# Optimization experiments

Measured on AMD Instinct MI355X. Metric: run time of the kernel, lower is better.

## Reference

```python
import jax, jax.numpy as jnp
import numpy as np

NUM_SUBNETS = 64
IN, HID, OUT = 6, 4, 2   # hard-coded in SubNetwork(6, 4, 2)
GHID = 6                 # GatingNetwork(6, 6, num_subnets)
BATCH = 524288


def tanhshrink(x):
    return x - jnp.tanh(x)


def setup_inputs() -> dict:
    key = jax.random.key(0)
    ks = jax.random.split(key, 9)
    s = 0.5
    return {
        "x":    jax.random.normal(ks[0], (BATCH, IN), dtype=jnp.float32),
        # stacked per-subnet params: SubNetwork layer1 (6->4), layer2 (4->2)
        "W1":   jax.random.normal(ks[1], (NUM_SUBNETS, HID, IN), dtype=jnp.float32) * s,
        "b1":   jax.random.normal(ks[2], (NUM_SUBNETS, HID), dtype=jnp.float32) * s,
        "W2":   jax.random.normal(ks[3], (NUM_SUBNETS, OUT, HID), dtype=jnp.float32) * s,
        "b2":   jax.random.normal(ks[4], (NUM_SUBNETS, OUT), dtype=jnp.float32) * s,
        # gating network: 6 -> 6 -> num_subnets
        "Gw1":  jax.random.normal(ks[5], (GHID, IN), dtype=jnp.float32) * s,
        "Gb1":  jax.random.normal(ks[6], (GHID,), dtype=jnp.float32) * s,
        "Gw2":  jax.random.normal(ks[7], (NUM_SUBNETS, GHID), dtype=jnp.float32) * s,
        "Gb2":  jax.random.normal(ks[8], (NUM_SUBNETS,), dtype=jnp.float32) * s,
    }


def reference(x, W1, b1, W2, b2, Gw1, Gb1, Gw2, Gb2):
    # All subnet MLPs fused across the subnet axis s (batched over b):
    h = tanhshrink(jnp.einsum('bi,shi->bsh', x, W1) + b1)          # [B, S, HID]
    outs = jnp.tanh(jnp.einsum('bsh,soh->bso', h, W2) + b2)       # [B, S, OUT]
    # Gating MLP; Softmax(dim=0) on an unbatched vector == softmax over subnets per sample
    g = tanhshrink(jnp.einsum('bi,hi->bh', x, Gw1) + Gb1)          # [B, GHID]
    gate = jax.nn.softmax(jnp.einsum('bh,sh->bs', g, Gw2) + Gb2, axis=-1)  # [B, S]
    # gate_weights @ outputs
    return jnp.einsum('bs,bso->bo', gate, outs)                    # [B, OUT]
```

## Files before the change

kernel.cpp:

```cpp
#include <hip/hip_runtime.h>


#define NSUB 64
#define L2E  1.4426950408889634f
#define L2E2 2.8853900817779268f

typedef float v2f __attribute__((ext_vector_type(2)));

__device__ __forceinline__ v2f pk_fma(v2f a, v2f b, v2f c) {
    return __builtin_elementwise_fma(a, b, c);
}
__device__ __forceinline__ v2f sp(float s) { return v2f{s, s}; }

__device__ __forceinline__ v2f sig_u(v2f z) {
    v2f e;
    e.x = __builtin_amdgcn_exp2f(z.x);
    e.y = __builtin_amdgcn_exp2f(z.y);
    v2f ep = e + 1.0f;
    v2f u;
    u.x = __builtin_amdgcn_rcpf(ep.x);
    u.y = __builtin_amdgcn_rcpf(ep.y);
    return u;
}

__device__ __forceinline__ float tanhshrink_s(float a) {
    float e = __builtin_amdgcn_exp2f(a * L2E2);
    float r = __builtin_amdgcn_rcpf(e + 1.0f);
    return fmaf(2.0f, r, a - 1.0f);
}

__global__ void pack_kernel(const float* __restrict__ W1, const float* __restrict__ b1,
                            const float* __restrict__ W2, const float* __restrict__ b2,
                            const float* __restrict__ Gw2, const float* __restrict__ Gb2,
                            float* __restrict__ ws)
{
    int p = threadIdx.x;
    if (p >= 32) return;
    int sa = p, sb = p + 32;
    float* f = ws + p * 128;
    for (int i = 0; i < 24; ++i) { f[2*i]   = W1[sa*24+i]*L2E2;  f[2*i+1]   = W1[sb*24+i]*L2E2; }
    for (int i = 0; i < 4;  ++i) { f[48+2*i] = b1[sa*4+i]*L2E2;  f[48+2*i+1] = b1[sb*4+i]*L2E2; }
    for (int i = 0; i < 8;  ++i) { f[56+2*i] = W2[sa*8+i];       f[56+2*i+1] = W2[sb*8+i]; }
    for (int i = 0; i < 8;  ++i) { f[72+2*i] = W2[sa*8+i]*(2.0f*L2E2);
                                   f[72+2*i+1] = W2[sb*8+i]*(2.0f*L2E2); }
    for (int o = 0; o < 2; ++o) {
        float rsA = 0.f, rsB = 0.f;
        for (int j = 0; j < 4; ++j) { rsA += W2[sa*8+o*4+j]; rsB += W2[sb*8+o*4+j]; }
        f[88+2*o]   = (b2[sa*2+o] - rsA) * L2E2;
        f[88+2*o+1] = (b2[sb*2+o] - rsB) * L2E2;
    }
    for (int i = 0; i < 6;  ++i) { f[92+2*i] = Gw2[sa*6+i]*L2E;  f[92+2*i+1] = Gw2[sb*6+i]*L2E; }
    f[104] = Gb2[sa]*L2E; f[105] = Gb2[sb]*L2E;
    for (int i = 106; i < 128; ++i) f[i] = 0.f;
}

__global__ __launch_bounds__(256) void moe_kernel(
    const float* __restrict__ x,
    const float* __restrict__ wpack,
    const float* __restrict__ Gw1, const float* __restrict__ Gb1,
    float* __restrict__ out)
{
    long t = blockIdx.x * blockDim.x + threadIdx.x;

    const float2* xv = (const float2*)(x + t * 6);
    float2 p0 = xv[0];
    float2 p1 = xv[1];
    float2 p2 = xv[2];
    float xs[6] = {p0.x, p0.y, p1.x, p1.y, p2.x, p2.y};

    float ga[6];
#pragma unroll
    for (int j = 0; j < 6; ++j) {
        float s = Gb1[j];
#pragma unroll
        for (int i = 0; i < 6; ++i)
            s = fmaf(Gw1[j * 6 + i], xs[i], s);
        ga[j] = tanhshrink_s(s);
    }

    v2f xa[6], gab[6];
#pragma unroll
    for (int i = 0; i < 6; ++i) xa[i] = sp(xs[i]);
#pragma unroll
    for (int j = 0; j < 6; ++j) gab[j] = sp(ga[j]);

    v2f accE = sp(0.f), accU0 = sp(0.f), accU1 = sp(0.f);

#pragma unroll 2
    for (int p = 0; p < 32; ++p) {
        const v2f* f2 = (const v2f*)(wpack + p * 128);

        v2f s0 = pk_fma(f2[0],  xa[0], f2[24]);
        v2f s1 = pk_fma(f2[6],  xa[0], f2[25]);
        v2f s2 = pk_fma(f2[12], xa[0], f2[26]);
        v2f s3 = pk_fma(f2[18], xa[0], f2[27]);
#pragma unroll
        for (int i = 1; i < 6; ++i) {
            s0 = pk_fma(f2[i],      xa[i], s0);
            s1 = pk_fma(f2[6 + i],  xa[i], s1);
            s2 = pk_fma(f2[12 + i], xa[i], s2);
            s3 = pk_fma(f2[18 + i], xa[i], s3);
        }

        v2f u0 = sig_u(s0);
        v2f u1 = sig_u(s1);
        v2f u2 = sig_u(s2);
        v2f u3 = sig_u(s3);

        v2f q0 = pk_fma(f2[28], s0, f2[44]);
        q0 = pk_fma(f2[29], s1, q0);
        q0 = pk_fma(f2[30], s2, q0);
        q0 = pk_fma(f2[31], s3, q0);
        q0 = pk_fma(f2[36], u0, q0);
        q0 = pk_fma(f2[37], u1, q0);
        q0 = pk_fma(f2[38], u2, q0);
        q0 = pk_fma(f2[39], u3, q0);

        v2f q1 = pk_fma(f2[32], s0, f2[45]);
        q1 = pk_fma(f2[33], s1, q1);
        q1 = pk_fma(f2[34], s2, q1);
        q1 = pk_fma(f2[35], s3, q1);
        q1 = pk_fma(f2[40], u0, q1);
        q1 = pk_fma(f2[41], u1, q1);
        q1 = pk_fma(f2[42], u2, q1);
        q1 = pk_fma(f2[43], u3, q1);

        v2f uo0 = sig_u(q0);
        v2f uo1 = sig_u(q1);

        v2f la = pk_fma(f2[46], gab[0], f2[52]);
        la = pk_fma(f2[47], gab[1], la);
        la = pk_fma(f2[48], gab[2], la);
        la = pk_fma(f2[49], gab[3], la);
        la = pk_fma(f2[50], gab[4], la);
        la = pk_fma(f2[51], gab[5], la);
        v2f ea;
        ea.x = __builtin_amdgcn_exp2f(la.x);
        ea.y = __builtin_amdgcn_exp2f(la.y);

        accE  = accE + ea;
        accU0 = pk_fma(ea, uo0, accU0);
        accU1 = pk_fma(ea, uo1, accU1);
    }

    float E  = accE.x + accE.y;
    float r  = __builtin_amdgcn_rcpf(E);
    float U0 = accU0.x + accU0.y;
    float U1 = accU1.x + accU1.y;
    float2 res;
    res.x = fmaf(-2.0f * U0, r, 1.0f);
    res.y = fmaf(-2.0f * U1, r, 1.0f);
    ((float2*)&out[t * 2])[0] = res;
}

extern "C" void kernel_launch(void* const* d_in, const int* in_sizes, int n_in,
                              void* d_out, int out_size, void* d_ws, size_t ws_size,
                              hipStream_t stream) {
    const float* x   = (const float*)d_in[0];
    const float* W1  = (const float*)d_in[1];
    const float* b1  = (const float*)d_in[2];
    const float* W2  = (const float*)d_in[3];
    const float* b2  = (const float*)d_in[4];
    const float* Gw1 = (const float*)d_in[5];
    const float* Gb1 = (const float*)d_in[6];
    const float* Gw2 = (const float*)d_in[7];
    const float* Gb2 = (const float*)d_in[8];
    float* out = (float*)d_out;
    float* ws  = (float*)d_ws;

    pack_kernel<<<1, 64, 0, stream>>>(W1, b1, W2, b2, Gw2, Gb2, ws);

    const int threads = 256;
    const int blocks = 524288 / threads;
    moe_kernel<<<blocks, threads, 0, stream>>>(x, ws, Gw1, Gb1, out);
}
```

Baseline: 68.48 us.

## Process four samples per thread to amortize packed weight loads

Each thread now handles four batch rows, loading x with float4 vector loads and writing outputs as float4. Every packed subnet weight fetched in the 32-pair loop is reused across the four samples, cutting scalar or LDS weight-load traffic per sample and adding independent instruction streams for ILP. The gating layer is vectorized across sample pairs. The cost is more registers per thread, a quarter as many threads (512 blocks), and the loop unroll pragma has been dropped.

```diff
diff --git a/kernel.cpp b/kernel.cpp
--- a/kernel.cpp
+++ b/kernel.cpp
@@ -21,12 +21,6 @@
     u.x = __builtin_amdgcn_rcpf(ep.x);
     u.y = __builtin_amdgcn_rcpf(ep.y);
     return u;
-}
-
-__device__ __forceinline__ float tanhshrink_s(float a) {
-    float e = __builtin_amdgcn_exp2f(a * L2E2);
-    float r = __builtin_amdgcn_rcpf(e + 1.0f);
-    return fmaf(2.0f, r, a - 1.0f);
 }
 
 __global__ void pack_kernel(const float* __restrict__ W1, const float* __restrict__ b1,
@@ -54,6 +48,65 @@
     for (int i = 106; i < 128; ++i) f[i] = 0.f;
 }
 
+__device__ __forceinline__ void step(const v2f* __restrict__ f2,
+                                     const float* __restrict__ xs,
+                                     const float* __restrict__ ga,
+                                     v2f& accE, v2f& accU0, v2f& accU1)
+{
+    v2f s0 = pk_fma(f2[0],  sp(xs[0]), f2[24]);
+    v2f s1 = pk_fma(f2[6],  sp(xs[0]), f2[25]);
+    v2f s2 = pk_fma(f2[12], sp(xs[0]), f2[26]);
+    v2f s3 = pk_fma(f2[18], sp(xs[0]), f2[27]);
+#pragma unroll
+    for (int i = 1; i < 6; ++i) {
+        v2f xi = sp(xs[i]);
+        s0 = pk_fma(f2[i],      xi, s0);
+        s1 = pk_fma(f2[6 + i],  xi, s1);
+        s2 = pk_fma(f2[12 + i], xi, s2);
+        s3 = pk_fma(f2[18 + i], xi, s3);
+    }
+
+    v2f u0 = sig_u(s0);
+    v2f u1 = sig_u(s1);
+    v2f u2 = sig_u(s2);
+    v2f u3 = sig_u(s3);
+
+    v2f q0 = pk_fma(f2[28], s0, f2[44]);
+    q0 = pk_fma(f2[29], s1, q0);
+    q0 = pk_fma(f2[30], s2, q0);
+    q0 = pk_fma(f2[31], s3, q0);
+    q0 = pk_fma(f2[36], u0, q0);
+    q0 = pk_fma(f2[37], u1, q0);
+    q0 = pk_fma(f2[38], u2, q0);
+    q0 = pk_fma(f2[39], u3, q0);
+
+    v2f q1 = pk_fma(f2[32], s0, f2[45]);
+    q1 = pk_fma(f2[33], s1, q1);
+    q1 = pk_fma(f2[34], s2, q1);
+    q1 = pk_fma(f2[35], s3, q1);
+    q1 = pk_fma(f2[40], u0, q1);
+    q1 = pk_fma(f2[41], u1, q1);
+    q1 = pk_fma(f2[42], u2, q1);
+    q1 = pk_fma(f2[43], u3, q1);
+
+    v2f uo0 = sig_u(q0);
+    v2f uo1 = sig_u(q1);
+
+    v2f la = pk_fma(f2[46], sp(ga[0]), f2[52]);
+    la = pk_fma(f2[47], sp(ga[1]), la);
+    la = pk_fma(f2[48], sp(ga[2]), la);
+    la = pk_fma(f2[49], sp(ga[3]), la);
+    la = pk_fma(f2[50], sp(ga[4]), la);
+    la = pk_fma(f2[51], sp(ga[5]), la);
+    v2f ea;
+    ea.x = __builtin_amdgcn_exp2f(la.x);
+    ea.y = __builtin_amdgcn_exp2f(la.y);
+
+    accE  = accE + ea;
+    accU0 = pk_fma(ea, uo0, accU0);
+    accU1 = pk_fma(ea, uo1, accU1);
+}
+
 __global__ __launch_bounds__(256) void moe_kernel(
     const float* __restrict__ x,
     const float* __restrict__ wpack,
@@ -62,95 +115,65 @@
 {
     long t = blockIdx.x * blockDim.x + threadIdx.x;
 
-    const float2* xv = (const float2*)(x + t * 6);
-    float2 p0 = xv[0];
-    float2 p1 = xv[1];
-    float2 p2 = xv[2];
-    float xs[6] = {p0.x, p0.y, p1.x, p1.y, p2.x, p2.y};
+    const float4* xv = (const float4*)(x + t * 24);
+    float4 v0 = xv[0], v1 = xv[1], v2 = xv[2], v3 = xv[3], v4 = xv[4], v5 = xv[5];
+    float xs[4][6] = {
+        {v0.x, v0.y, v0.z, v0.w, v1.x, v1.y},
+        {v1.z, v1.w, v2.x, v2.y, v2.z, v2.w},
+        {v3.x, v3.y, v3.z, v3.w, v4.x, v4.y},
+        {v4.z, v4.w, v5.x, v5.y, v5.z, v5.w},
+    };
 
-    float ga[6];
+    float ga[4][6];
 #pragma unroll
     for (int j = 0; j < 6; ++j) {
-        float s = Gb1[j];
+        v2f sP = sp(Gb1[j]), sQ = sP;
 #pragma unroll
-        for (int i = 0; i < 6; ++i)
-            s = fmaf(Gw1[j * 6 + i], xs[i], s);
-        ga[j] = tanhshrink_s(s);
+        for (int i = 0; i < 6; ++i) {
+            v2f w = sp(Gw1[j * 6 + i]);
+            sP = pk_fma(w, v2f{xs[0][i], xs[1][i]}, sP);
+            sQ = pk_fma(w, v2f{xs[2][i], xs[3][i]}, sQ);
+        }
+        v2f uP = sig_u(sP * L2E2);
+        v2f uQ = sig_u(sQ * L2E2);
+        v2f gP = pk_fma(sp(2.0f), uP, sP - 1.0f);
+        v2f gQ = pk_fma(sp(2.0f), uQ, sQ - 1.0f);
+        ga[0][j] = gP.x; ga[1][j] = gP.y;
+        ga[2][j] = gQ.x; ga[3][j] = gQ.y;
     }
 
-    v2f xa[6], gab[6];
+    v2f accE[4], U0[4], U1[4];
 #pragma unroll
-    for (int i = 0; i < 6; ++i) xa[i] = sp(xs[i]);
-#pragma unroll
-    for (int j = 0; j < 6; ++j) gab[j] = sp(ga[j]);
+    for (int k = 0; k < 4; ++k) { accE[k] = sp(0.f); U0[k] = sp(0.f); U1[k] = sp(0.f); }
 
-    v2f accE = sp(0.f), accU0 = sp(0.f), accU1 = sp(0.f);
-
-#pragma unroll 2
     for (int p = 0; p < 32; ++p) {
         const v2f* f2 = (const v2f*)(wpack + p * 128);
-
-        v2f s0 = pk_fma(f2[0],  xa[0], f2[24]);
-        v2f s1 = pk_fma(f2[6],  xa[0], f2[25]);
-        v2f s2 = pk_fma(f2[12], xa[0], f2[26]);
-        v2f s3 = pk_fma(f2[18], xa[0], f2[27]);
-#pragma unroll
-        for (int i = 1; i < 6; ++i) {
-            s0 = pk_fma(f2[i],      xa[i], s0);
-            s1 = pk_fma(f2[6 + i],  xa[i], s1);
-            s2 = pk_fma(f2[12 + i], xa[i], s2);
-            s3 = pk_fma(f2[18 + i], xa[i], s3);
-        }
-
-        v2f u0 = sig_u(s0);
-        v2f u1 = sig_u(s1);
-        v2f u2 = sig_u(s2);
-        v2f u3 = sig_u(s3);
-
-        v2f q0 = pk_fma(f2[28], s0, f2[44]);
-        q0 = pk_fma(f2[29], s1, q0);
-        q0 = pk_fma(f2[30], s2, q0);
-        q0 = pk_fma(f2[31], s3, q0);
-        q0 = pk_fma(f2[36], u0, q0);
-        q0 = pk_fma(f2[37], u1, q0);
-        q0 = pk_fma(f2[38], u2, q0);
-        q0 = pk_fma(f2[39], u3, q0);
-
-        v2f q1 = pk_fma(f2[32], s0, f2[45]);
-        q1 = pk_fma(f2[33], s1, q1);
-        q1 = pk_fma(f2[34], s2, q1);
-        q1 = pk_fma(f2[35], s3, q1);
-        q1 = pk_fma(f2[40], u0, q1);
-        q1 = pk_fma(f2[41], u1, q1);
-        q1 = pk_fma(f2[42], u2, q1);
-        q1 = pk_fma(f2[43], u3, q1);
-
-        v2f uo0 = sig_u(q0);
-        v2f uo1 = sig_u(q1);
-
-        v2f la = pk_fma(f2[46], gab[0], f2[52]);
-        la = pk_fma(f2[47], gab[1], la);
-        la = pk_fma(f2[48], gab[2], la);
-        la = pk_fma(f2[49], gab[3], la);
-        la = pk_fma(f2[50], gab[4], la);
-        la = pk_fma(f2[51], gab[5], la);
-        v2f ea;
-        ea.x = __builtin_amdgcn_exp2f(la.x);
-        ea.y = __builtin_amdgcn_exp2f(la.y);
-
-        accE  = accE + ea;
-        accU0 = pk_fma(ea, uo0, accU0);
-        accU1 = pk_fma(ea, uo1, accU1);
+        step(f2, xs[0], ga[0], accE[0], U0[0], U1[0]);
+        step(f2, xs[1], ga[1], accE[1], U0[1], U1[1]);
+        step(f2, xs[2], ga[2], accE[2], U0[2], U1[2]);
+        step(f2, xs[3], ga[3], accE[3], U0[3], U1[3]);
     }
 
-    float E  = accE.x + accE.y;
-    float r  = __builtin_amdgcn_rcpf(E);
-    float U0 = accU0.x + accU0.y;
-    float U1 = accU1.x + accU1.y;
-    float2 res;
-    res.x = fmaf(-2.0f * U0, r, 1.0f);
-    res.y = fmaf(-2.0f * U1, r, 1.0f);
-    ((float2*)&out[t * 2])[0] = res;
+    float4 r0, r1;
+    {
+        float E0 = accE[0].x + accE[0].y, E1 = accE[1].x + accE[1].y;
+        float c0 = __builtin_amdgcn_rcpf(E0), c1 = __builtin_amdgcn_rcpf(E1);
+        r0.x = fmaf(-2.0f * (U0[0].x + U0[0].y), c0, 1.0f);
+        r0.y = fmaf(-2.0f * (U1[0].x + U1[0].y), c0, 1.0f);
+        r0.z = fmaf(-2.0f * (U0[1].x + U0[1].y), c1, 1.0f);
+        r0.w = fmaf(-2.0f * (U1[1].x + U1[1].y), c1, 1.0f);
+    }
+    {
+        float E2 = accE[2].x + accE[2].y, E3 = accE[3].x + accE[3].y;
+        float c2 = __builtin_amdgcn_rcpf(E2), c3 = __builtin_amdgcn_rcpf(E3);
+        r1.x = fmaf(-2.0f * (U0[2].x + U0[2].y), c2, 1.0f);
+        r1.y = fmaf(-2.0f * (U1[2].x + U1[2].y), c2, 1.0f);
+        r1.z = fmaf(-2.0f * (U0[3].x + U0[3].y), c3, 1.0f);
+        r1.w = fmaf(-2.0f * (U1[3].x + U1[3].y), c3, 1.0f);
+    }
+    float4* op = (float4*)&out[t * 8];
+    op[0] = r0;
+    op[1] = r1;
 }
 
 extern "C" void kernel_launch(void* const* d_in, const int* in_sizes, int n_in,
@@ -171,6 +194,6 @@
     pack_kernel<<<1, 64, 0, stream>>>(W1, b1, W2, b2, Gw2, Gb2, ws);
 
     const int threads = 256;
-    const int blocks = 524288 / threads;
+    const int blocks = (524288 / 4) / threads;
     moe_kernel<<<blocks, threads, 0, stream>>>(x, ws, Gw1, Gb1, out);
 }
```

After: 65.56 us. -4.3%, faster.
